# Optimization experiments

Measured on AMD Instinct MI355X. Metric: run time of the kernel, lower is better.

## Reference

```python
import jax, jax.numpy as jnp
import numpy as np


def _conv(x, w, b=None):
    # x: [B,C,H,W], w: [O,I,kh,kw], 'same' padding for odd kernels
    pad_h = (w.shape[2] - 1) // 2
    pad_w = (w.shape[3] - 1) // 2
    y = jax.lax.conv_general_dilated(
        x, w, window_strides=(1, 1),
        padding=[(pad_h, pad_h), (pad_w, pad_w)],
        dimension_numbers=("NCHW", "OIHW", "NCHW"))
    if b is not None:
        y = y + b[None, :, None, None]
    return y


def setup_inputs() -> dict:
    key = jax.random.key(0)
    ks = jax.random.split(key, 14)
    B, L_I, L_H, MAZE, F, OUT = 32, 8, 128, 64, 5, 16
    s = 0.05  # weight scale
    return {
        "X": jax.random.normal(ks[0], (B, L_I, MAZE, MAZE), jnp.float32),
        "hid_w": jax.random.normal(ks[1], (L_H, L_I, 3, 3), jnp.float32) * s,
        "hid_b": jax.random.normal(ks[2], (L_H,), jnp.float32) * s,
        "h0_w": jax.random.normal(ks[3], (L_H, L_H, 3, 3), jnp.float32) * s,
        "h0_b": jax.random.normal(ks[4], (L_H,), jnp.float32) * s,
        "c0_w": jax.random.normal(ks[5], (L_H, L_H, 3, 3), jnp.float32) * s,
        "c0_b": jax.random.normal(ks[6], (L_H,), jnp.float32) * s,
        "conv_w": jax.random.normal(ks[7], (1, L_H, F, F), jnp.float32) * s,
        "conv_b": jax.random.normal(ks[8], (1,), jnp.float32) * s,
        "W_ih": jax.random.normal(ks[9], (4 * L_H, 1), jnp.float32) * s,
        "W_hh": jax.random.normal(ks[10], (4 * L_H, L_H), jnp.float32) * s,
        "b_ih": jnp.zeros((4 * L_H,), jnp.float32),
        "b_hh": jnp.zeros((4 * L_H,), jnp.float32),
        "policy_w": jax.random.normal(ks[11], (OUT, L_H, 1, 1), jnp.float32) * s,
        "k": 10,
    }


def reference(X, hid_w, hid_b, h0_w, h0_b, c0_w, c0_b, conv_w, conv_b,
              W_ih, W_hh, b_ih, b_hh, policy_w, k):
    # hid: [B, l_h, H, W]
    hid = _conv(X, hid_w, hid_b)
    # torch .transpose(1,3).view(-1,l_h): keep as [B, W, H, l_h]
    h = jnp.transpose(_conv(hid, h0_w, h0_b), (0, 3, 2, 1))
    c = jnp.transpose(_conv(hid, c0_w, c0_b), (0, 3, 2, 1))
    bias = b_ih + b_hh

    def step(carry, _):
        h, c = carry
        h_map = jnp.transpose(h, (0, 3, 2, 1))          # [B, l_h, H, W]
        inp = jnp.transpose(_conv(h_map, conv_w, conv_b), (0, 3, 2, 1))  # [B,W,H,1]
        # PyTorch LSTMCell gate order: i, f, g, o
        gates = inp @ W_ih.T + h @ W_hh.T + bias        # [B, W, H, 4*l_h]
        i, f, g, o = jnp.split(gates, 4, axis=-1)
        c_new = jax.nn.sigmoid(f) * c + jax.nn.sigmoid(i) * jnp.tanh(g)
        h_new = jax.nn.sigmoid(o) * jnp.tanh(c_new)
        return (h_new, c_new), None

    (h, c), _ = jax.lax.scan(step, (h, c), None, length=k - 1)
    hk = jnp.transpose(h, (0, 3, 2, 1))                 # [B, l_h, H, W]
    logits = _conv(hk, policy_w, None)                  # 1x1 conv, no bias
    return logits
```

## Files before the change

### kernel.cpp

```cpp
#include <hip/hip_runtime.h>
#include <math.h>


typedef _Float16 f16;
typedef _Float16 f16x8 __attribute__((ext_vector_type(8)));
typedef float    f32x4 __attribute__((ext_vector_type(4)));

#define NB 32
#define HWD 64
#define NPIX (NB*HWD*HWD)

#define OB_CC    ((size_t)0)
#define OB_HA    ((size_t)67108864)
#define OB_HB    ((size_t)100663296)
#define OB_DA    ((size_t)134217728)
#define OB_DB    ((size_t)142606336)
#define OB_WCB   ((size_t)150994944)
#define OB_WGB   ((size_t)151584768)
#define OB_WIB   ((size_t)151715840)
#define OB_W5B   ((size_t)151748608)
#define OB_WHB   ((size_t)151756800)
#define OB_BS2   ((size_t)151781376)
#define WS_BYTES ((size_t)151783424)

__device__ __forceinline__ float sigm(float x){ return 1.f/(1.f+__expf(-x)); }
__device__ __forceinline__ float tanhx(float x){ return 1.f - 2.f/(1.f+__expf(2.f*x)); }

__global__ void kTrans(const float* __restrict__ h0w, const float* __restrict__ c0w,
                       const float* __restrict__ whh, const float* __restrict__ cw5,
                       const float* __restrict__ wih, const float* __restrict__ hw,
                       const float* __restrict__ bih, const float* __restrict__ bhh,
                       const float* __restrict__ cb,
                       f16* __restrict__ wcb, f16* __restrict__ wgb,
                       f16* __restrict__ wib, f16* __restrict__ w5b,
                       f16* __restrict__ whb, float* __restrict__ bs2)
{
    int e = blockIdx.x*256 + threadIdx.x;
    if (e < 294912) {
        int j = e & 7, l = (e >> 3) & 63, kk = (e >> 9) & 3;
        int nt = (e >> 11) & 15, tap = e >> 15;
        int c = (nt & 7)*16 + (l & 15);
        int k = kk*32 + (l >> 4)*8 + j;
        const float* src = (nt < 8) ? h0w : c0w;
        wcb[e] = (f16)src[((size_t)c*128 + k)*9 + tap];
    }
    if (e < 65536) {
        int j = e & 7, l = (e >> 3) & 63, fb = e >> 9;
        int nt = fb >> 2, kk = fb & 3;
        int cg = nt*16 + (l & 15), k = kk*32 + (l >> 4)*8 + j;
        wgb[e] = (f16)whh[(size_t)cg*128 + k];
    }
    if (e < 16384) {
        int l = (e >> 3) & 63, nt = e >> 9;
        wib[e] = (f16)wih[nt*16 + (l & 15)];
    }
    if (e < 12288) {
        int j = e & 7, l = (e >> 3) & 63, fb = e >> 9;
        int nt = fb/3, kk = fb - nt*3;
        int c = nt*16 + (l & 15), k = kk*32 + (l >> 4)*8 + j;
        whb[e] = (k < 72) ? (f16)hw[(size_t)c*72 + (k & 7)*9 + (k >> 3)] : (f16)0.f;
    }
    if (e < 4096) {
        int j = e & 7, l = (e >> 3) & 63, fb = e >> 9;
        int nt = fb >> 2, kk = fb & 3;
        int n = nt*16 + (l & 15), k = kk*32 + (l >> 4)*8 + j;
        w5b[e] = (n < 25) ? (f16)cw5[k*25 + n] : (f16)0.f;
    }
    if (e < 512) bs2[e] = bih[e] + bhh[e] + cb[0]*wih[e];
}

__global__ __launch_bounds__(256,2) void kInit(const float* __restrict__ X,
                                               const f16* __restrict__ whb,
                                               const float* __restrict__ hidb,
                                               const f16* __restrict__ wcb,
                                               const f16* __restrict__ w5b,
                                               const float* __restrict__ h0b,
                                               const float* __restrict__ c0b,
                                               f16* __restrict__ h0out,
                                               float* __restrict__ cc,
                                               f16* __restrict__ dout)
{
    __shared__ f16 sX[1536];
    __shared__ f16 sHalo[100*128];
    int t = threadIdx.x;
    int blk = blockIdx.x;
    int b = blk >> 6, ti = (blk >> 3) & 7, tj = blk & 7;
    int i0 = ti*8, j0 = tj*8;
    int l = t & 63, wn = t >> 6;

    for (int e = t; e < 1536; e += 256) {
        if (e < 1152) {
            int ci = e/144, pos = e - ci*144;
            int gi = i0 + pos/12 - 2, gj = j0 + pos%12 - 2;
            float xv = 0.f;
            if ((unsigned)gi < 64u && (unsigned)gj < 64u)
                xv = X[(((size_t)b*8 + ci)*64 + gi)*64 + gj];
            sX[pos*8 + ci] = (f16)xv;
        } else {
            sX[e] = (f16)0.f;
        }
    }
    __syncthreads();

    for (int mt = wn; mt < 7; mt += 4) {
        int m = mt*16 + (l & 15);
        int pi = m/10, pj = m - pi*10;
        f16x8 ax[3];
        #pragma unroll
        for (int kk = 0; kk < 3; ++kk) {
            int tap = kk*4 + (l >> 4);
            int dy = tap/3, dx = tap - dy*3;
            ax[kk] = *(const f16x8*)&sX[((pi + dy)*12 + (pj + dx))*8];
        }
        #pragma unroll
        for (int nt = 0; nt < 8; ++nt) {
            f32x4 hc = {0.f,0.f,0.f,0.f};
            #pragma unroll
            for (int kk = 0; kk < 3; ++kk)
                hc = __builtin_amdgcn_mfma_f32_16x16x32_f16(ax[kk],
                        *(const f16x8*)(whb + ((size_t)(nt*3 + kk)*64 + l)*8), hc, 0, 0, 0);
            int c = nt*16 + (l & 15);
            float bv = hidb[c];
            #pragma unroll
            for (int r = 0; r < 4; ++r) {
                int m2 = mt*16 + (l >> 4)*4 + r;
                if (m2 < 100) {
                    int pi2 = m2/10, pj2 = m2 - pi2*10;
                    int gi = i0 + pi2 - 1, gj = j0 + pj2 - 1;
                    bool inb = ((unsigned)gi < 64u && (unsigned)gj < 64u);
                    sHalo[(m2*16 + ((c >> 3) ^ (m2 & 7)))*8 + (c & 7)] =
                        inb ? (f16)(hc[r] + bv) : (f16)0.f;
                }
            }
        }
    }
    __syncthreads();

    f32x4 acc[4][4];
    #pragma unroll
    for (int mi = 0; mi < 4; ++mi)
        #pragma unroll
        for (int q = 0; q < 4; ++q) acc[mi][q] = (f32x4){0.f,0.f,0.f,0.f};

    for (int tap = 0; tap < 9; ++tap) {
        int dy = tap/3, dx = tap - dy*3;
        f16x8 a[4][4];
        #pragma unroll
        for (int mi = 0; mi < 4; ++mi) {
            int mrow = mi*16 + (l & 15);
            int pos = ((mrow >> 3) + dy)*10 + (mrow & 7) + dx;
            #pragma unroll
            for (int kk = 0; kk < 4; ++kk)
                a[mi][kk] = *(const f16x8*)&sHalo[(pos*16 + ((kk*4 + (l >> 4)) ^ (pos & 7)))*8];
        }
        #pragma unroll
        for (int q = 0; q < 4; ++q) {
            int nt = wn*4 + q;
            f16x8 bf[4];
            #pragma unroll
            for (int kk = 0; kk < 4; ++kk)
                bf[kk] = *(const f16x8*)(wcb + ((size_t)((tap*16 + nt)*4 + kk)*64 + l)*8);
            #pragma unroll
            for (int mi = 0; mi < 4; ++mi)
                #pragma unroll
                for (int kk = 0; kk < 4; ++kk)
                    acc[mi][q] = __builtin_amdgcn_mfma_f32_16x16x32_f16(a[mi][kk], bf[kk], acc[mi][q], 0, 0, 0);
        }
    }

    __syncthreads();
    f16* sH = sHalo;

    int cl = l & 15;
    bool isC = (wn >= 2);
    #pragma unroll
    for (int q = 0; q < 4; ++q) {
        int c = ((wn & 1)*4 + q)*16 + cl;
        float bv = isC ? c0b[c] : h0b[c];
        #pragma unroll
        for (int mi = 0; mi < 4; ++mi) {
            int mbase = mi*16 + (l >> 4)*4;
            if (isC) {
                float4 cv;
                cv.x = acc[mi][q][0] + bv; cv.y = acc[mi][q][1] + bv;
                cv.z = acc[mi][q][2] + bv; cv.w = acc[mi][q][3] + bv;
                *(float4*)(cc + (size_t)blk*8192 + (size_t)c*64 + mbase) = cv;
            } else {
                #pragma unroll
                for (int r = 0; r < 4; ++r) {
                    int m = mbase + r;
                    sH[(m*16 + ((c >> 3) ^ (m & 7)))*8 + (c & 7)] = (f16)(acc[mi][q][r] + bv);
                }
            }
        }
    }
    __syncthreads();

    {
        int m0 = wn*16 + (l & 15);
        f16x8 av[4];
        #pragma unroll
        for (int kk = 0; kk < 4; ++kk)
            av[kk] = *(const f16x8*)&sH[(m0*16 + ((kk*4 + (l >> 4)) ^ (m0 & 7)))*8];
        #pragma unroll
        for (int nt = 0; nt < 2; ++nt) {
            f32x4 dc = {0.f,0.f,0.f,0.f};
            #pragma unroll
            for (int kk = 0; kk < 4; ++kk)
                dc = __builtin_amdgcn_mfma_f32_16x16x32_f16(av[kk],
                        *(const f16x8*)(w5b + ((size_t)((nt*4 + kk)*64 + l))*8), dc, 0, 0, 0);
            #pragma unroll
            for (int r = 0; r < 4; ++r) {
                int mm = wn*16 + (l >> 4)*4 + r;
                size_t gp = ((((size_t)b*64 + i0 + (mm >> 3))*64 + j0 + (mm & 7))*32) + nt*16 + (l & 15);
                dout[gp] = (f16)dc[r];
            }
        }
    }
    for (int e = t; e < 1024; e += 256) {
        int pos = e >> 4, ch = e & 15;
        f16x8 v = *(const f16x8*)&sH[(pos*16 + (ch ^ (pos & 7)))*8];
        *(f16x8*)(h0out + ((((size_t)b*64 + i0 + (pos >> 3))*64 + j0 + (pos & 7))*128) + ch*8) = v;
    }
}

__global__ __launch_bounds__(256,4) void kFuse(const f16* __restrict__ hin,
                                               const f16* __restrict__ din,
                                               const f16* __restrict__ wgb,
                                               const f16* __restrict__ wib,
                                               const f16* __restrict__ w5b,
                                               const float* __restrict__ bs2,
                                               float* __restrict__ cc,
                                               f16* __restrict__ hout,
                                               f16* __restrict__ dout)
{
    __shared__ f16 sDH[144*32];
    __shared__ f16 sH[64*128];
    int t = threadIdx.x;
    int blk = blockIdx.x;
    int b = blk >> 6, ti = (blk >> 3) & 7, tj = blk & 7;
    int i0 = ti*8, j0 = tj*8;
    int l = t & 63, w = t >> 6;
    int wn = w >> 1, wm = w & 1;
    int cl = l & 15;

    f16x8 a[2][4];
    #pragma unroll
    for (int mi = 0; mi < 2; ++mi) {
        int m = (wm + mi*2)*16 + (l & 15);
        size_t gp = (((size_t)b*64 + i0 + (m >> 3))*64 + j0 + (m & 7))*128;
        #pragma unroll
        for (int kk = 0; kk < 4; ++kk)
            a[mi][kk] = *(const f16x8*)(hin + gp + kk*32 + (l >> 4)*8);
    }
    float4 coldv[4][2];
    #pragma unroll
    for (int q = 0; q < 4; ++q)
        #pragma unroll
        for (int mi = 0; mi < 2; ++mi) {
            int c = (wn*4 + q)*16 + cl;
            int mbase = (wm + mi*2)*16 + (l >> 4)*4;
            coldv[q][mi] = *(const float4*)(cc + (size_t)blk*8192 + (size_t)c*64 + mbase);
        }
    for (int e = t; e < 576; e += 256) {
        int pos = e >> 2, ch = e & 3;
        int gi = i0 + pos/12 - 2, gj = j0 + pos%12 - 2;
        f16x8 v = {0,0,0,0,0,0,0,0};
        if ((unsigned)gi < 64u && (unsigned)gj < 64u)
            v = *(const f16x8*)(din + (((size_t)b*64 + gi)*64 + gj)*32 + ch*8);
        *(f16x8*)&sDH[pos*32 + ch*8] = v;
    }
    __syncthreads();

    f16x8 adh[2];
    #pragma unroll
    for (int mi = 0; mi < 2; ++mi) {
        int m = (wm + mi*2)*16 + (l & 15);
        int pi = m >> 3, pj = m & 7;
        f16 tmp[8];
        #pragma unroll
        for (int j = 0; j < 8; ++j) {
            int kp = (l >> 4)*8 + j;
            int kpc = (kp < 25) ? kp : 0;
            int ty = kpc/5, tx = kpc - ty*5;
            f16 v = sDH[((pi + ty)*12 + (pj + tx))*32 + kpc];
            tmp[j] = (kp < 25) ? v : (f16)0.f;
        }
        adh[mi] = *(f16x8*)tmp;
    }

    bool doD = (dout != nullptr);
    #pragma unroll
    for (int q = 0; q < 4; ++q) {
        f32x4 acc2[2][4];
        #pragma unroll
        for (int mi = 0; mi < 2; ++mi)
            #pragma unroll
            for (int g = 0; g < 4; ++g) acc2[mi][g] = (f32x4){0.f,0.f,0.f,0.f};
        #pragma unroll
        for (int g = 0; g < 4; ++g) {
            int nt = g*8 + wn*4 + q;
            #pragma unroll
            for (int kk = 0; kk < 4; ++kk) {
                f16x8 bf = *(const f16x8*)(wgb + ((size_t)((nt*4 + kk)*64 + l))*8);
                #pragma unroll
                for (int mi = 0; mi < 2; ++mi)
                    acc2[mi][g] = __builtin_amdgcn_mfma_f32_16x16x32_f16(a[mi][kk], bf, acc2[mi][g], 0, 0, 0);
            }
            f16x8 be = *(const f16x8*)(wib + ((size_t)(nt*64 + l))*8);
            #pragma unroll
            for (int mi = 0; mi < 2; ++mi)
                acc2[mi][g] = __builtin_amdgcn_mfma_f32_16x16x32_f16(adh[mi], be, acc2[mi][g], 0, 0, 0);
        }
        int c = (wn*4 + q)*16 + cl;
        float bi = bs2[c], bff = bs2[128 + c], bg = bs2[256 + c], bo = bs2[384 + c];
        #pragma unroll
        for (int mi = 0; mi < 2; ++mi) {
            int mbase = (wm + mi*2)*16 + (l >> 4)*4;
            size_t cbase = (size_t)blk*8192 + (size_t)c*64 + mbase;
            const float* cp = (const float*)&coldv[q][mi];
            float cn[4], hn[4];
            #pragma unroll
            for (int r = 0; r < 4; ++r) {
                float vi = acc2[mi][0][r] + bi;
                float vf = acc2[mi][1][r] + bff;
                float vg = acc2[mi][2][r] + bg;
                float vo = acc2[mi][3][r] + bo;
                float cv = sigm(vf)*cp[r] + sigm(vi)*tanhx(vg);
                cn[r] = cv;
                hn[r] = sigm(vo)*tanhx(cv);
            }
            *(float4*)(cc + cbase) = make_float4(cn[0], cn[1], cn[2], cn[3]);
            #pragma unroll
            for (int r = 0; r < 4; ++r) {
                int m = mbase + r;
                sH[(m*16 + ((c >> 3) ^ (m & 7)))*8 + (c & 7)] = (f16)hn[r];
            }
        }
    }

    __syncthreads();
    if (doD) {
        int m0 = w*16 + (l & 15);
        f16x8 av[4];
        #pragma unroll
        for (int kk = 0; kk < 4; ++kk)
            av[kk] = *(const f16x8*)&sH[(m0*16 + ((kk*4 + (l >> 4)) ^ (m0 & 7)))*8];
        #pragma unroll
        for (int nt = 0; nt < 2; ++nt) {
            f32x4 dc = {0.f,0.f,0.f,0.f};
            #pragma unroll
            for (int kk = 0; kk < 4; ++kk)
                dc = __builtin_amdgcn_mfma_f32_16x16x32_f16(av[kk],
                        *(const f16x8*)(w5b + ((size_t)((nt*4 + kk)*64 + l))*8), dc, 0, 0, 0);
            #pragma unroll
            for (int r = 0; r < 4; ++r) {
                int mm = w*16 + (l >> 4)*4 + r;
                size_t gp = ((((size_t)b*64 + i0 + (mm >> 3))*64 + j0 + (mm & 7))*32) + nt*16 + (l & 15);
                dout[gp] = (f16)dc[r];
            }
        }
    }
    for (int e = t; e < 1024; e += 256) {
        int pos = e >> 4, ch = e & 15;
        f16x8 v = *(const f16x8*)&sH[(pos*16 + (ch ^ (pos & 7)))*8];
        *(f16x8*)(hout + ((((size_t)b*64 + i0 + (pos >> 3))*64 + j0 + (pos & 7))*128) + ch*8) = v;
    }
}

__global__ __launch_bounds__(256) void kPolicy(const f16* __restrict__ h,
                                               const float* __restrict__ pw,
                                               float* __restrict__ out)
{
    __shared__ float Ps[16*128];
    int t = threadIdx.x;
    for (int e = t; e < 2048; e += 256) Ps[e] = pw[e];
    __syncthreads();
    size_t pid = (size_t)blockIdx.x*256 + t;
    int b = (int)(pid >> 12), rem = (int)(pid & 4095);
    float acc[16];
    #pragma unroll
    for (int o = 0; o < 16; ++o) acc[o] = 0.f;
    const f16x8* hb8 = (const f16x8*)(h + pid*128);
    #pragma unroll 2
    for (int k8 = 0; k8 < 16; ++k8) {
        f16x8 hv = hb8[k8];
        float hf[8];
        #pragma unroll
        for (int e = 0; e < 8; ++e) hf[e] = (float)hv[e];
        #pragma unroll
        for (int o = 0; o < 16; ++o) {
            float4 w0 = *(const float4*)&Ps[o*128 + k8*8];
            float4 w1 = *(const float4*)&Ps[o*128 + k8*8 + 4];
            acc[o] += hf[0]*w0.x + hf[1]*w0.y + hf[2]*w0.z + hf[3]*w0.w
                    + hf[4]*w1.x + hf[5]*w1.y + hf[6]*w1.z + hf[7]*w1.w;
        }
    }
    #pragma unroll
    for (int o = 0; o < 16; ++o)
        out[((size_t)b*16 + o)*4096 + rem] = acc[o];
}

extern "C" void kernel_launch(void* const* d_in, const int* in_sizes, int n_in,
                              void* d_out, int out_size, void* d_ws, size_t ws_size,
                              hipStream_t stream) {
    const float* X      = (const float*)d_in[0];
    const float* hid_w  = (const float*)d_in[1];
    const float* hid_b  = (const float*)d_in[2];
    const float* h0_w   = (const float*)d_in[3];
    const float* h0_b   = (const float*)d_in[4];
    const float* c0_w   = (const float*)d_in[5];
    const float* c0_b   = (const float*)d_in[6];
    const float* conv_w = (const float*)d_in[7];
    const float* conv_b = (const float*)d_in[8];
    const float* W_ih   = (const float*)d_in[9];
    const float* W_hh   = (const float*)d_in[10];
    const float* b_ih   = (const float*)d_in[11];
    const float* b_hh   = (const float*)d_in[12];
    const float* pol_w  = (const float*)d_in[13];

    if (ws_size < WS_BYTES) return;

    char* wsb = (char*)d_ws;
    float* CC  = (float*)(wsb + OB_CC);
    f16*   HA  = (f16*)  (wsb + OB_HA);
    f16*   HB  = (f16*)  (wsb + OB_HB);
    f16*   DA  = (f16*)  (wsb + OB_DA);
    f16*   DB  = (f16*)  (wsb + OB_DB);
    f16*   WCB = (f16*)  (wsb + OB_WCB);
    f16*   WGB = (f16*)  (wsb + OB_WGB);
    f16*   WIB = (f16*)  (wsb + OB_WIB);
    f16*   W5B = (f16*)  (wsb + OB_W5B);
    f16*   WHB = (f16*)  (wsb + OB_WHB);
    float* BS2 = (float*)(wsb + OB_BS2);

    kTrans<<<1152, 256, 0, stream>>>(h0_w, c0_w, W_hh, conv_w, W_ih, hid_w,
                                     b_ih, b_hh, conv_b,
                                     WCB, WGB, WIB, W5B, WHB, BS2);
    kInit<<<2048, 256, 0, stream>>>(X, WHB, hid_b, WCB, W5B, h0_b, c0_b, HA, CC, DA);
    for (int st = 0; st < 9; ++st) {
        const f16* hin = (st & 1) ? HB : HA;
        const f16* din = (st & 1) ? DB : DA;
        f16* hout      = (st & 1) ? HA : HB;
        f16* dout      = (st & 1) ? DA : DB;
        if (st == 8) dout = nullptr;
        kFuse<<<2048, 256, 0, stream>>>(hin, din, WGB, WIB, W5B, BS2, CC, hout, dout);
    }
    kPolicy<<<512, 256, 0, stream>>>(HB, pol_w, (float*)d_out);
}
```

Before: 900.6 us.

## Store LSTM cell state in fp16 and fuse policy conv into last step

The cell state buffer drops from fp32 to fp16, halving its read and write traffic in every recurrent step. The final step no longer writes c, h or the conv map. It computes the 1x1 policy conv with MFMA from shared memory and writes the logits directly, which removes the separate kPolicy launch and its re-read of h. Keeping c in fp16 across nine steps adds rounding error to the recurrence.

```diff
diff --git a/kernel.cpp b/kernel.cpp
--- a/kernel.cpp
+++ b/kernel.cpp
@@ -3,25 +3,26 @@
 
 
 typedef _Float16 f16;
+typedef _Float16 f16x4 __attribute__((ext_vector_type(4)));
 typedef _Float16 f16x8 __attribute__((ext_vector_type(8)));
 typedef float    f32x4 __attribute__((ext_vector_type(4)));
 
 #define NB 32
 #define HWD 64
-#define NPIX (NB*HWD*HWD)
 
 #define OB_CC    ((size_t)0)
-#define OB_HA    ((size_t)67108864)
-#define OB_HB    ((size_t)100663296)
-#define OB_DA    ((size_t)134217728)
-#define OB_DB    ((size_t)142606336)
-#define OB_WCB   ((size_t)150994944)
-#define OB_WGB   ((size_t)151584768)
-#define OB_WIB   ((size_t)151715840)
-#define OB_W5B   ((size_t)151748608)
-#define OB_WHB   ((size_t)151756800)
-#define OB_BS2   ((size_t)151781376)
-#define WS_BYTES ((size_t)151783424)
+#define OB_HA    ((size_t)33554432)
+#define OB_HB    ((size_t)67108864)
+#define OB_DA    ((size_t)100663296)
+#define OB_DB    ((size_t)109051904)
+#define OB_WCB   ((size_t)117440512)
+#define OB_WGB   ((size_t)118030336)
+#define OB_WIB   ((size_t)118161408)
+#define OB_W5B   ((size_t)118194176)
+#define OB_WHB   ((size_t)118202368)
+#define OB_WPB   ((size_t)118226944)
+#define OB_BS2   ((size_t)118231040)
+#define WS_BYTES ((size_t)118233088)
 
 __device__ __forceinline__ float sigm(float x){ return 1.f/(1.f+__expf(-x)); }
 __device__ __forceinline__ float tanhx(float x){ return 1.f - 2.f/(1.f+__expf(2.f*x)); }
@@ -29,11 +30,13 @@
 __global__ void kTrans(const float* __restrict__ h0w, const float* __restrict__ c0w,
                        const float* __restrict__ whh, const float* __restrict__ cw5,
                        const float* __restrict__ wih, const float* __restrict__ hw,
+                       const float* __restrict__ polw,
                        const float* __restrict__ bih, const float* __restrict__ bhh,
                        const float* __restrict__ cb,
                        f16* __restrict__ wcb, f16* __restrict__ wgb,
                        f16* __restrict__ wib, f16* __restrict__ w5b,
-                       f16* __restrict__ whb, float* __restrict__ bs2)
+                       f16* __restrict__ whb, f16* __restrict__ wpb,
+                       float* __restrict__ bs2)
 {
     int e = blockIdx.x*256 + threadIdx.x;
     if (e < 294912) {
@@ -66,6 +69,11 @@
         int n = nt*16 + (l & 15), k = kk*32 + (l >> 4)*8 + j;
         w5b[e] = (n < 25) ? (f16)cw5[k*25 + n] : (f16)0.f;
     }
+    if (e < 2048) {
+        int j = e & 7, l = (e >> 3) & 63, kk = e >> 9;
+        int o = l & 15, k = kk*32 + (l >> 4)*8 + j;
+        wpb[e] = (f16)polw[(size_t)o*128 + k];
+    }
     if (e < 512) bs2[e] = bih[e] + bhh[e] + cb[0]*wih[e];
 }
 
@@ -77,7 +85,7 @@
                                                const float* __restrict__ h0b,
                                                const float* __restrict__ c0b,
                                                f16* __restrict__ h0out,
-                                               float* __restrict__ cc,
+                                               f16* __restrict__ cc,
                                                f16* __restrict__ dout)
 {
     __shared__ f16 sX[1536];
@@ -181,10 +189,10 @@
         for (int mi = 0; mi < 4; ++mi) {
             int mbase = mi*16 + (l >> 4)*4;
             if (isC) {
-                float4 cv;
-                cv.x = acc[mi][q][0] + bv; cv.y = acc[mi][q][1] + bv;
-                cv.z = acc[mi][q][2] + bv; cv.w = acc[mi][q][3] + bv;
-                *(float4*)(cc + (size_t)blk*8192 + (size_t)c*64 + mbase) = cv;
+                f16x4 cv;
+                #pragma unroll
+                for (int r = 0; r < 4; ++r) cv[r] = (f16)(acc[mi][q][r] + bv);
+                *(f16x4*)(cc + (size_t)blk*8192 + (size_t)c*64 + mbase) = cv;
             } else {
                 #pragma unroll
                 for (int r = 0; r < 4; ++r) {
@@ -229,10 +237,12 @@
                                                const f16* __restrict__ wgb,
                                                const f16* __restrict__ wib,
                                                const f16* __restrict__ w5b,
+                                               const f16* __restrict__ wpb,
                                                const float* __restrict__ bs2,
-                                               float* __restrict__ cc,
+                                               f16* __restrict__ cc,
                                                f16* __restrict__ hout,
-                                               f16* __restrict__ dout)
+                                               f16* __restrict__ dout,
+                                               float* __restrict__ outp)
 {
     __shared__ f16 sDH[144*32];
     __shared__ f16 sH[64*128];
@@ -243,6 +253,7 @@
     int l = t & 63, w = t >> 6;
     int wn = w >> 1, wm = w & 1;
     int cl = l & 15;
+    bool doPol = (outp != nullptr);
 
     f16x8 a[2][4];
     #pragma unroll
@@ -253,14 +264,14 @@
         for (int kk = 0; kk < 4; ++kk)
             a[mi][kk] = *(const f16x8*)(hin + gp + kk*32 + (l >> 4)*8);
     }
-    float4 coldv[4][2];
+    f16x4 coldv[4][2];
     #pragma unroll
     for (int q = 0; q < 4; ++q)
         #pragma unroll
         for (int mi = 0; mi < 2; ++mi) {
             int c = (wn*4 + q)*16 + cl;
             int mbase = (wm + mi*2)*16 + (l >> 4)*4;
-            coldv[q][mi] = *(const float4*)(cc + (size_t)blk*8192 + (size_t)c*64 + mbase);
+            coldv[q][mi] = *(const f16x4*)(cc + (size_t)blk*8192 + (size_t)c*64 + mbase);
         }
     for (int e = t; e < 576; e += 256) {
         int pos = e >> 2, ch = e & 3;
@@ -289,7 +300,6 @@
         adh[mi] = *(f16x8*)tmp;
     }
 
-    bool doD = (dout != nullptr);
     #pragma unroll
     for (int q = 0; q < 4; ++q) {
         f32x4 acc2[2][4];
@@ -317,8 +327,6 @@
         #pragma unroll
         for (int mi = 0; mi < 2; ++mi) {
             int mbase = (wm + mi*2)*16 + (l >> 4)*4;
-            size_t cbase = (size_t)blk*8192 + (size_t)c*64 + mbase;
-            const float* cp = (const float*)&coldv[q][mi];
             float cn[4], hn[4];
             #pragma unroll
             for (int r = 0; r < 4; ++r) {
@@ -326,11 +334,16 @@
                 float vf = acc2[mi][1][r] + bff;
                 float vg = acc2[mi][2][r] + bg;
                 float vo = acc2[mi][3][r] + bo;
-                float cv = sigm(vf)*cp[r] + sigm(vi)*tanhx(vg);
+                float cv = sigm(vf)*(float)coldv[q][mi][r] + sigm(vi)*tanhx(vg);
                 cn[r] = cv;
                 hn[r] = sigm(vo)*tanhx(cv);
             }
-            *(float4*)(cc + cbase) = make_float4(cn[0], cn[1], cn[2], cn[3]);
+            if (!doPol) {
+                f16x4 cf;
+                #pragma unroll
+                for (int r = 0; r < 4; ++r) cf[r] = (f16)cn[r];
+                *(f16x4*)(cc + (size_t)blk*8192 + (size_t)c*64 + mbase) = cf;
+            }
             #pragma unroll
             for (int r = 0; r < 4; ++r) {
                 int m = mbase + r;
@@ -340,7 +353,7 @@
     }
 
     __syncthreads();
-    if (doD) {
+    if (!doPol) {
         int m0 = w*16 + (l & 15);
         f16x8 av[4];
         #pragma unroll
@@ -360,45 +373,29 @@
                 dout[gp] = (f16)dc[r];
             }
         }
-    }
-    for (int e = t; e < 1024; e += 256) {
-        int pos = e >> 4, ch = e & 15;
-        f16x8 v = *(const f16x8*)&sH[(pos*16 + (ch ^ (pos & 7)))*8];
-        *(f16x8*)(hout + ((((size_t)b*64 + i0 + (pos >> 3))*64 + j0 + (pos & 7))*128) + ch*8) = v;
-    }
-}
-
-__global__ __launch_bounds__(256) void kPolicy(const f16* __restrict__ h,
-                                               const float* __restrict__ pw,
-                                               float* __restrict__ out)
-{
-    __shared__ float Ps[16*128];
-    int t = threadIdx.x;
-    for (int e = t; e < 2048; e += 256) Ps[e] = pw[e];
-    __syncthreads();
-    size_t pid = (size_t)blockIdx.x*256 + t;
-    int b = (int)(pid >> 12), rem = (int)(pid & 4095);
-    float acc[16];
-    #pragma unroll
-    for (int o = 0; o < 16; ++o) acc[o] = 0.f;
-    const f16x8* hb8 = (const f16x8*)(h + pid*128);
-    #pragma unroll 2
-    for (int k8 = 0; k8 < 16; ++k8) {
-        f16x8 hv = hb8[k8];
-        float hf[8];
-        #pragma unroll
-        for (int e = 0; e < 8; ++e) hf[e] = (float)hv[e];
-        #pragma unroll
-        for (int o = 0; o < 16; ++o) {
-            float4 w0 = *(const float4*)&Ps[o*128 + k8*8];
-            float4 w1 = *(const float4*)&Ps[o*128 + k8*8 + 4];
-            acc[o] += hf[0]*w0.x + hf[1]*w0.y + hf[2]*w0.z + hf[3]*w0.w
-                    + hf[4]*w1.x + hf[5]*w1.y + hf[6]*w1.z + hf[7]*w1.w;
-        }
-    }
-    #pragma unroll
-    for (int o = 0; o < 16; ++o)
-        out[((size_t)b*16 + o)*4096 + rem] = acc[o];
+        for (int e = t; e < 1024; e += 256) {
+            int pos = e >> 4, ch = e & 15;
+            f16x8 v = *(const f16x8*)&sH[(pos*16 + (ch ^ (pos & 7)))*8];
+            *(f16x8*)(hout + ((((size_t)b*64 + i0 + (pos >> 3))*64 + j0 + (pos & 7))*128) + ch*8) = v;
+        }
+    } else {
+        int m0 = w*16 + (l & 15);
+        f16x8 av[4];
+        #pragma unroll
+        for (int kk = 0; kk < 4; ++kk)
+            av[kk] = *(const f16x8*)&sH[(m0*16 + ((kk*4 + (l >> 4)) ^ (m0 & 7)))*8];
+        f32x4 pc = {0.f,0.f,0.f,0.f};
+        #pragma unroll
+        for (int kk = 0; kk < 4; ++kk)
+            pc = __builtin_amdgcn_mfma_f32_16x16x32_f16(av[kk],
+                    *(const f16x8*)(wpb + ((size_t)(kk*64 + l))*8), pc, 0, 0, 0);
+        int o = l & 15;
+        #pragma unroll
+        for (int r = 0; r < 4; ++r) {
+            int mm = w*16 + (l >> 4)*4 + r;
+            outp[(((size_t)b*16 + o)*4096) + (size_t)(i0 + (mm >> 3))*64 + j0 + (mm & 7)] = pc[r];
+        }
+    }
 }
 
 extern "C" void kernel_launch(void* const* d_in, const int* in_sizes, int n_in,
@@ -422,7 +419,7 @@
     if (ws_size < WS_BYTES) return;
 
     char* wsb = (char*)d_ws;
-    float* CC  = (float*)(wsb + OB_CC);
+    f16*   CC  = (f16*)  (wsb + OB_CC);
     f16*   HA  = (f16*)  (wsb + OB_HA);
     f16*   HB  = (f16*)  (wsb + OB_HB);
     f16*   DA  = (f16*)  (wsb + OB_DA);
@@ -432,19 +429,20 @@
     f16*   WIB = (f16*)  (wsb + OB_WIB);
     f16*   W5B = (f16*)  (wsb + OB_W5B);
     f16*   WHB = (f16*)  (wsb + OB_WHB);
+    f16*   WPB = (f16*)  (wsb + OB_WPB);
     float* BS2 = (float*)(wsb + OB_BS2);
 
-    kTrans<<<1152, 256, 0, stream>>>(h0_w, c0_w, W_hh, conv_w, W_ih, hid_w,
+    kTrans<<<1152, 256, 0, stream>>>(h0_w, c0_w, W_hh, conv_w, W_ih, hid_w, pol_w,
                                      b_ih, b_hh, conv_b,
-                                     WCB, WGB, WIB, W5B, WHB, BS2);
+                                     WCB, WGB, WIB, W5B, WHB, WPB, BS2);
     kInit<<<2048, 256, 0, stream>>>(X, WHB, hid_b, WCB, W5B, h0_b, c0_b, HA, CC, DA);
     for (int st = 0; st < 9; ++st) {
         const f16* hin = (st & 1) ? HB : HA;
         const f16* din = (st & 1) ? DB : DA;
         f16* hout      = (st & 1) ? HA : HB;
         f16* dout      = (st & 1) ? DA : DB;
-        if (st == 8) dout = nullptr;
-        kFuse<<<2048, 256, 0, stream>>>(hin, din, WGB, WIB, W5B, BS2, CC, hout, dout);
-    }
-    kPolicy<<<512, 256, 0, stream>>>(HB, pol_w, (float*)d_out);
+        float* outp    = (st == 8) ? (float*)d_out : nullptr;
+        kFuse<<<2048, 256, 0, stream>>>(hin, din, WGB, WIB, W5B, WPB, BS2,
+                                        CC, hout, dout, outp);
+    }
 }
```

Result: faster. 809.0 us (-10.2%).
